# Kernel tuning notes

Measured on AMD Instinct MI355X. Metric: run time of the kernel, lower is better.

The kernel has to match this reference:

```python
import jax, jax.numpy as jnp
import numpy as np

N, W, MAX_DEPTH = 250_000, 784, 16
N_NODES = 2 ** MAX_DEPTH + 1  # 65537
DEPTH = MAX_DEPTH - 1  # deepest traversal that keeps indices in-range


def setup_inputs() -> dict:
    key = jax.random.key(0)
    k1, k2, k3 = jax.random.split(key, 3)
    x = jax.random.randint(k1, (N, W), 0, 2, dtype=jnp.int32)  # binary features
    node_choices = jax.random.randint(k2, (N_NODES,), 0, W, dtype=jnp.int32)
    node_predictions = jax.random.randint(k3, (N_NODES,), 0, 2).astype(jnp.float32)
    return {"x": x, "node_choices": node_choices,
            "node_predictions": node_predictions, "depth": DEPTH}


def reference(x, node_choices, node_predictions, depth):
    # Sequential decision-tree traversal: at each level gather the split
    # feature index for every sample's current node, read that feature bit,
    # and descend to child 2*n+1 (bit=0) or 2*n+2 (bit=1).
    n = x.shape[0]
    nodes0 = jnp.zeros((n,), dtype=jnp.int32)

    def body(_, nodes):
        choices = node_choices[nodes]                                   # [n]
        decisions = jnp.take_along_axis(x, choices[:, None].astype(jnp.int32), axis=1)[:, 0]
        return nodes * 2 + decisions + 1

    nodes = jax.lax.fori_loop(0, depth, body, nodes0)
    return node_predictions[nodes].astype(jnp.bool_)
```

## Files before the change

kernel.cpp:

```cpp
#include <hip/hip_runtime.h>


template <int NSEG_C, int TAIL_C>
__global__ __launch_bounds__(256) void pack_kernel(
    const int* __restrict__ x,
    unsigned*  __restrict__ packed,
    int n, int w, int nseg_rt, int tail_rt, int wpr)
{
    const int  gtid = blockIdx.x * blockDim.x + threadIdx.x;
    const int  wave = gtid >> 6;
    const int  lane = gtid & 63;
    const long long row0 = (long long)wave * 4;

    const int nseg = NSEG_C ? NSEG_C : nseg_rt;
    const int tail = NSEG_C ? TAIL_C : tail_rt;

    #pragma unroll
    for (int rr = 0; rr < 4; ++rr) {
        const long long r = row0 + rr;
        if (r >= n) return;
        const int* __restrict__ rowp = x + r * (long long)w;
        unsigned*  __restrict__ outp = packed + r * (long long)wpr;

        #pragma unroll
        for (int seg = 0; seg < nseg; ++seg) {
            const int v = rowp[(seg << 6) + lane];
            const unsigned long long m = __ballot(v != 0);
            if (lane < 2)
                outp[(seg << 1) + lane] = (unsigned)(m >> (lane << 5));
        }
        if (tail) {
            const int v = (lane < tail) ? rowp[(nseg << 6) + lane] : 0;
            const unsigned long long m = __ballot(v != 0);
            if (lane < 2 && (lane << 5) < tail)
                outp[(nseg << 1) + lane] = (unsigned)(m >> (lane << 5));
        }
    }
}

__global__ __launch_bounds__(256) void traverse_kernel(
    const unsigned* __restrict__ packed,
    const int*      __restrict__ choices,
    const float*    __restrict__ preds,
    const int*      __restrict__ depth_p,
    int*            __restrict__ out,
    int n, int wpr)
{
    const int i = blockIdx.x * blockDim.x + threadIdx.x;
    if (i >= n) return;

    const unsigned* __restrict__ row = packed + (long long)i * wpr;
    const int depth = *depth_p;

    int node = 0;
    for (int d = 0; d < depth; ++d) {
        const int c = choices[node];
        const unsigned bits = row[c >> 5];
        node = (node << 1) + (int)((bits >> (c & 31)) & 1u) + 1;
    }
    out[i] = (preds[node] != 0.0f) ? 1 : 0;
}

__global__ __launch_bounds__(256) void direct_kernel(
    const int*   __restrict__ x,
    const int*   __restrict__ choices,
    const float* __restrict__ preds,
    const int*   __restrict__ depth_p,
    int*         __restrict__ out,
    int n, int w)
{
    const int i = blockIdx.x * blockDim.x + threadIdx.x;
    if (i >= n) return;
    const int depth = *depth_p;
    const int* __restrict__ row = x + (long long)i * (long long)w;
    int node = 0;
    for (int d = 0; d < depth; ++d) {
        const int c   = choices[node];
        const int bit = row[c];
        node = node * 2 + bit + 1;
    }
    out[i] = (preds[node] != 0.0f) ? 1 : 0;
}

extern "C" void kernel_launch(void* const* d_in, const int* in_sizes, int n_in,
                              void* d_out, int out_size, void* d_ws, size_t ws_size,
                              hipStream_t stream) {
    const int*   x       = (const int*)d_in[0];
    const int*   choices = (const int*)d_in[1];
    const float* preds   = (const float*)d_in[2];
    const int*   depth_p = (const int*)d_in[3];
    int*         out     = (int*)d_out;

    const int n = out_size;
    const int w = in_sizes[0] / n;

    const int wpr = (w + 31) / 32;
    const size_t need = (size_t)n * wpr * sizeof(unsigned);

    if (ws_size < need) {
        const int block = 256;
        const int grid  = (n + block - 1) / block;
        direct_kernel<<<grid, block, 0, stream>>>(x, choices, preds, depth_p,
                                                  out, n, w);
        return;
    }

    unsigned* packed = (unsigned*)d_ws;

    {
        const int block = 256;
        const long long waves = ((long long)n + 3) / 4;
        const long long grid  = (waves + 3) / 4;
        const int nseg = w >> 6, tail = w & 63;
        if (w == 784)
            pack_kernel<12, 16><<<dim3((unsigned)grid), block, 0, stream>>>(
                x, packed, n, w, nseg, tail, wpr);
        else
            pack_kernel<0, 0><<<dim3((unsigned)grid), block, 0, stream>>>(
                x, packed, n, w, nseg, tail, wpr);
    }

    {
        const int block = 256;
        const int grid  = (n + block - 1) / block;
        traverse_kernel<<<grid, block, 0, stream>>>(packed, choices, preds,
                                                    depth_p, out, n, wpr);
    }
}
```

Measured before the change: 1.077 ms.

## Stage tree tables and per-block feature bits in LDS for traversal

New measurement: 1.085 ms. No clear change (+0.8%).

```diff
diff --git a/kernel.cpp b/kernel.cpp
--- a/kernel.cpp
+++ b/kernel.cpp
@@ -1,64 +1,121 @@
 #include <hip/hip_runtime.h>
 
 
-template <int NSEG_C, int TAIL_C>
+#define WPR 25
+#define CH_LDS 16384
+
+__global__ __launch_bounds__(256) void pack_tables_kernel(
+    const int*   __restrict__ choices,
+    const float* __restrict__ preds,
+    const int*   __restrict__ depth_p,
+    unsigned short* __restrict__ ch16,
+    unsigned*       __restrict__ predbits)
+{
+    const int t = threadIdx.x;
+    if (blockIdx.x < 128) {
+        const int j = blockIdx.x * 256 + t;
+        ch16[j] = (unsigned short)choices[j];
+    } else {
+        const int b = (blockIdx.x - 128) * 256 + t;
+        const int depth = *depth_p;
+        const int base  = (1 << depth) - 1;
+        const int count = 1 << depth;
+        const int v = (b < count) ? (preds[base + b] != 0.0f) : 0;
+        const unsigned long long m = __ballot(v != 0);
+        const int lane = t & 63;
+        if (lane < 2) {
+            const int word = ((b >> 6) << 1) + lane;
+            if (word < 1024)
+                predbits[word] = (unsigned)(m >> (lane << 5));
+        }
+    }
+}
+
 __global__ __launch_bounds__(256) void pack_kernel(
     const int* __restrict__ x,
     unsigned*  __restrict__ packed,
-    int n, int w, int nseg_rt, int tail_rt, int wpr)
+    int n, int w)
 {
+    constexpr int NSEG = 12, TAIL = 16;
     const int  gtid = blockIdx.x * blockDim.x + threadIdx.x;
     const int  wave = gtid >> 6;
     const int  lane = gtid & 63;
     const long long row0 = (long long)wave * 4;
-
-    const int nseg = NSEG_C ? NSEG_C : nseg_rt;
-    const int tail = NSEG_C ? TAIL_C : tail_rt;
 
     #pragma unroll
     for (int rr = 0; rr < 4; ++rr) {
         const long long r = row0 + rr;
         if (r >= n) return;
         const int* __restrict__ rowp = x + r * (long long)w;
-        unsigned*  __restrict__ outp = packed + r * (long long)wpr;
+        unsigned*  __restrict__ outp = packed + (r >> 8) * (WPR * 256) + (r & 255);
 
         #pragma unroll
-        for (int seg = 0; seg < nseg; ++seg) {
+        for (int seg = 0; seg < NSEG; ++seg) {
             const int v = rowp[(seg << 6) + lane];
             const unsigned long long m = __ballot(v != 0);
             if (lane < 2)
-                outp[(seg << 1) + lane] = (unsigned)(m >> (lane << 5));
+                outp[((seg << 1) + lane) * 256] = (unsigned)(m >> (lane << 5));
         }
-        if (tail) {
-            const int v = (lane < tail) ? rowp[(nseg << 6) + lane] : 0;
+        {
+            const int v = (lane < TAIL) ? rowp[(NSEG << 6) + lane] : 0;
             const unsigned long long m = __ballot(v != 0);
-            if (lane < 2 && (lane << 5) < tail)
-                outp[(nseg << 1) + lane] = (unsigned)(m >> (lane << 5));
+            if (lane == 0)
+                outp[(2 * NSEG) * 256] = (unsigned)m;
         }
     }
 }
 
-__global__ __launch_bounds__(256) void traverse_kernel(
-    const unsigned* __restrict__ packed,
-    const int*      __restrict__ choices,
-    const float*    __restrict__ preds,
-    const int*      __restrict__ depth_p,
-    int*            __restrict__ out,
-    int n, int wpr)
+__global__ __launch_bounds__(256) void traverse_lds_kernel(
+    const unsigned*       __restrict__ packed,
+    const unsigned short* __restrict__ ch16,
+    const unsigned*       __restrict__ predbits,
+    const int*            __restrict__ choices,
+    const float*          __restrict__ preds,
+    const int*            __restrict__ depth_p,
+    int* __restrict__ out, int n)
 {
-    const int i = blockIdx.x * blockDim.x + threadIdx.x;
+    __shared__ unsigned short ch[CH_LDS];
+    __shared__ unsigned bits[WPR * 256];
+    __shared__ unsigned pb[1024];
+
+    const int tid = threadIdx.x;
+    const long long blockRow0 = (long long)blockIdx.x * 256;
+    const int depth = *depth_p;
+
+    {
+        const unsigned* __restrict__ src = (const unsigned*)ch16;
+        unsigned* dst = (unsigned*)ch;
+        #pragma unroll
+        for (int k = 0; k < 32; ++k)
+            dst[k * 256 + tid] = src[k * 256 + tid];
+    }
+    #pragma unroll
+    for (int k = 0; k < 4; ++k)
+        pb[k * 256 + tid] = predbits[k * 256 + tid];
+    {
+        const unsigned* __restrict__ src = packed + (long long)blockIdx.x * (WPR * 256);
+        #pragma unroll
+        for (int k = 0; k < WPR; ++k)
+            bits[k * 256 + tid] = src[k * 256 + tid];
+    }
+    __syncthreads();
+
+    const long long i = blockRow0 + tid;
     if (i >= n) return;
-
-    const unsigned* __restrict__ row = packed + (long long)i * wpr;
-    const int depth = *depth_p;
 
     int node = 0;
     for (int d = 0; d < depth; ++d) {
-        const int c = choices[node];
-        const unsigned bits = row[c >> 5];
-        node = (node << 1) + (int)((bits >> (c & 31)) & 1u) + 1;
+        const int c = (node < CH_LDS - 1) ? (int)ch[node] : choices[node];
+        const unsigned wv = bits[(c >> 5) * 256 + tid];
+        node = (node << 1) + (int)((wv >> (c & 31)) & 1u) + 1;
     }
-    out[i] = (preds[node] != 0.0f) ? 1 : 0;
+
+    if (depth <= 15) {
+        const int idx = node - ((1 << depth) - 1);
+        out[i] = (int)((pb[idx >> 5] >> (idx & 31)) & 1u);
+    } else {
+        out[i] = (preds[node] != 0.0f) ? 1 : 0;
+    }
 }
 
 __global__ __launch_bounds__(256) void direct_kernel(
@@ -94,10 +151,13 @@
     const int n = out_size;
     const int w = in_sizes[0] / n;
 
-    const int wpr = (w + 31) / 32;
-    const size_t need = (size_t)n * wpr * sizeof(unsigned);
+    const long long nblk = (n + 255) / 256;
+    const size_t bits_bytes = (size_t)nblk * WPR * 256 * sizeof(unsigned);
+    const size_t ch16_off   = (bits_bytes + 255) & ~(size_t)255;
+    const size_t pb_off     = ch16_off + 32768 * sizeof(unsigned short);
+    const size_t need       = pb_off + 1024 * sizeof(unsigned);
 
-    if (ws_size < need) {
+    if (w != 784 || ws_size < need) {
         const int block = 256;
         const int grid  = (n + block - 1) / block;
         direct_kernel<<<grid, block, 0, stream>>>(x, choices, preds, depth_p,
@@ -105,25 +165,17 @@
         return;
     }
 
-    unsigned* packed = (unsigned*)d_ws;
+    unsigned*       packed   = (unsigned*)d_ws;
+    unsigned short* ch16     = (unsigned short*)((char*)d_ws + ch16_off);
+    unsigned*       predbits = (unsigned*)((char*)d_ws + pb_off);
 
+    pack_tables_kernel<<<256, 256, 0, stream>>>(choices, preds, depth_p,
+                                                ch16, predbits);
     {
-        const int block = 256;
         const long long waves = ((long long)n + 3) / 4;
         const long long grid  = (waves + 3) / 4;
-        const int nseg = w >> 6, tail = w & 63;
-        if (w == 784)
-            pack_kernel<12, 16><<<dim3((unsigned)grid), block, 0, stream>>>(
-                x, packed, n, w, nseg, tail, wpr);
-        else
-            pack_kernel<0, 0><<<dim3((unsigned)grid), block, 0, stream>>>(
-                x, packed, n, w, nseg, tail, wpr);
+        pack_kernel<<<dim3((unsigned)grid), 256, 0, stream>>>(x, packed, n, w);
     }
-
-    {
-        const int block = 256;
-        const int grid  = (n + block - 1) / block;
-        traverse_kernel<<<grid, block, 0, stream>>>(packed, choices, preds,
-                                                    depth_p, out, n, wpr);
-    }
+    traverse_lds_kernel<<<dim3((unsigned)nblk), 256, 0, stream>>>(
+        packed, ch16, predbits, choices, preds, depth_p, out, n);
 }
```
